# Kernel tuning notes

Measured on AMD Instinct MI355X. Metric: run time of the kernel, lower is better.

The kernel has to match this reference:

```python
import jax, jax.numpy as jnp
import numpy as np

N_NODES = 20000
N_EDGES = 640000
IN_DIM = 256
HID = 128
N_GRAPHS = 64


def setup_inputs() -> dict:
    key = jax.random.key(0)
    ks = jax.random.split(key, 9)
    x = jax.random.normal(ks[0], (N_NODES, IN_DIM), jnp.float32)
    edge_index = jax.random.randint(ks[1], (2, N_EDGES), 0, N_NODES, dtype=jnp.int32)
    batch = jnp.sort(jax.random.randint(ks[2], (N_NODES,), 0, N_GRAPHS, dtype=jnp.int32))

    def lin(k, fan_in, fan_out):
        # torch.nn.Linear default init: U(-1/sqrt(fan_in), 1/sqrt(fan_in))
        bound = 1.0 / np.sqrt(fan_in)
        kw, kb = jax.random.split(k)
        W = jax.random.uniform(kw, (fan_in, fan_out), jnp.float32, -bound, bound)
        b = jax.random.uniform(kb, (fan_out,), jnp.float32, -bound, bound)
        return W, b

    W0, b0 = lin(ks[3], IN_DIM, HID)
    W1, b1 = lin(ks[4], HID, HID)
    W2, b2 = lin(ks[5], HID, HID)
    return dict(x=x, edge_index=edge_index, batch=batch,
                W0=W0, b0=b0, W1=W1, b1=b1, W2=W2, b2=b2)


def reference(x, edge_index, batch, W0, b0, W1, b1, W2, b2):
    src, dst = edge_index[0], edge_index[1]
    edge_batch = batch[src]  # [E] segment id per edge
    ones = jnp.ones((edge_batch.shape[0], 1), x.dtype)
    counts = jax.ops.segment_sum(ones, edge_batch, num_segments=N_GRAPHS)
    inv_counts = 1.0 / jnp.maximum(counts, 1.0)

    def pool(z):
        # gather endpoint features, concat -> [E, 2*HID], mean pool by graph
        edge_emb = jnp.concatenate([z[src], z[dst]], axis=1)
        return jax.ops.segment_sum(edge_emb, edge_batch, num_segments=N_GRAPHS) * inv_counts

    g = []
    z = x
    for W, b in ((W0, b0), (W1, b1), (W2, b2)):
        z = z @ W + b
        g.append(pool(z))
    return jnp.concatenate(g, axis=1)  # [N_GRAPHS, 3 * 2 * HID]
```

## Files before the change

kernel.cpp:

```cpp
#include <hip/hip_runtime.h>

#define N_NODES 20000
#define N_EDGES 640000
#define N_GRAPHS 64

#define NCHUNK 256
#define CHUNK_SZ 79
#define GSPLIT 8
#define GSUB 8

#define BG_TILE 2048
#define NBG 313
#define SEGCAP 80
#define GR_CAP 768
#define NSLOT4 (NBG * SEGCAP / 4)

#define CD_OFF      0
#define DEG_OFF     1280000
#define CNT_OFF     1300000
#define Y_OFF       1300064
#define PART_OFF    1316448
#define BH_OFF      5510752
#define VALS_OFF    5530784

__global__ __launch_bounds__(256) void bucket_g_k(const int* __restrict__ ei,
                                                  const int* __restrict__ batch,
                                                  unsigned* __restrict__ vals,
                                                  unsigned* __restrict__ bh,
                                                  float* __restrict__ Y) {
    __shared__ unsigned hist[N_GRAPHS];
    __shared__ unsigned base[N_GRAPHS + 1];
    __shared__ unsigned lv[BG_TILE];
    __shared__ unsigned char gidx[BG_TILE];
    const int t = threadIdx.x;
    const int blk = blockIdx.x;
    if (t < N_GRAPHS) hist[t] = 0u;
    __syncthreads();

    const int e0 = blk * BG_TILE;
    const int ecnt = (e0 + BG_TILE <= N_EDGES) ? BG_TILE : (N_EDGES - e0);
    unsigned pv[8], rnk[8], gg[8];
#pragma unroll
    for (int k = 0; k < 8; ++k) {
        int i = t + k * 256;
        if (i < ecnt) {
            unsigned s = (unsigned)ei[e0 + i];
            unsigned d = (unsigned)ei[N_EDGES + e0 + i];
            unsigned g = (unsigned)batch[s];
            pv[k] = (s << 15) | d;
            gg[k] = g;
            rnk[k] = atomicAdd(&hist[g], 1u);
        } else {
            gg[k] = 0xFFFFFFFFu;
        }
    }
    __syncthreads();
    if (t == 0) {
        unsigned acc = 0u;
        base[0] = 0u;
        for (int g = 0; g < N_GRAPHS; ++g) { acc += hist[g]; base[g + 1] = acc; }
    }
    if (t < N_GRAPHS) {
        unsigned c = hist[t];
        bh[blk * N_GRAPHS + t] = (c > SEGCAP) ? SEGCAP : c;
    }
    __syncthreads();
    if (t < N_GRAPHS) {
        unsigned b0 = base[t], b1 = base[t + 1];
        for (unsigned i = b0; i < b1; ++i) gidx[i] = (unsigned char)t;
    }
#pragma unroll
    for (int k = 0; k < 8; ++k) {
        if (gg[k] != 0xFFFFFFFFu) lv[base[gg[k]] + rnk[k]] = pv[k];
    }
    __syncthreads();
    for (int i = t; i < ecnt; i += 256) {
        unsigned g = gidx[i];
        unsigned slot = (unsigned)i - base[g];
        if (slot < SEGCAP)
            vals[((size_t)g * NBG + blk) * SEGCAP + slot] = lv[i];
    }
    if (blk == 0) {
        float4* y4 = (float4*)Y;
        for (int i = t; i < 64 * 64; i += 256) y4[i] = make_float4(0.f, 0.f, 0.f, 0.f);
    }
}

__global__ __launch_bounds__(1024) void cd_col_k(const unsigned* __restrict__ vals,
                                                 const unsigned* __restrict__ bh,
                                                 const int* __restrict__ batch,
                                                 float* __restrict__ Cdcol,
                                                 float* __restrict__ deg,
                                                 float* __restrict__ counts) {
    __shared__ unsigned scnt[NBG];
    __shared__ unsigned dh[2500];
    __shared__ unsigned sdeg[GR_CAP];
    __shared__ int s_lo, s_hi;
    const int t = threadIdx.x;
    const int g = blockIdx.x >> 2;
    const int q = blockIdx.x & 3;
    const int d0 = q * 5000;

    for (int i = t; i < 2500; i += 1024) dh[i] = 0u;
    if (t < NBG) scnt[t] = bh[t * N_GRAPHS + g];
    if (q == 0) {
        if (t < GR_CAP) sdeg[t] = 0u;
        if (t == 0) {
            int lo = 0, hi = N_NODES;
            while (lo < hi) { int m = (lo + hi) >> 1; if (batch[m] < g) lo = m + 1; else hi = m; }
            s_lo = lo;
            int lo2 = lo; hi = N_NODES;
            while (lo2 < hi) { int m = (lo2 + hi) >> 1; if (batch[m] < g + 1) lo2 = m + 1; else hi = m; }
            s_hi = lo2;
        }
    }
    __syncthreads();
    const int lo = (q == 0) ? s_lo : 0;

    const uint4* v4 = (const uint4*)(vals + (size_t)g * NBG * SEGCAP);
    for (int i = t; i < NSLOT4; i += 1024) {
        uint4 v = *(v4 + i);
        unsigned w = (unsigned)i * 4u;
        unsigned seg = (unsigned)(((unsigned long long)w * 53687092ull) >> 32);
        unsigned local = w - seg * 80u;
        unsigned c = scnt[seg];
#define CD_ONE(VX, L)                                                            \
        if ((L) < c) {                                                           \
            int rd_ = (int)((VX) & 0x7FFFu) - d0;                                \
            if ((unsigned)rd_ < 5000u)                                           \
                atomicAdd(&dh[rd_ >> 1], 1u << ((rd_ & 1) * 16));                \
            if (q == 0) {                                                        \
                int rs_ = (int)((VX) >> 15) - lo;                                \
                if ((unsigned)rs_ < (unsigned)GR_CAP) atomicAdd(&sdeg[rs_], 1u); \
            }                                                                    \
        }
        CD_ONE(v.x, local + 0u)
        CD_ONE(v.y, local + 1u)
        CD_ONE(v.z, local + 2u)
        CD_ONE(v.w, local + 3u)
#undef CD_ONE
    }
    __syncthreads();

    float2* outc = (float2*)(Cdcol + (size_t)g * N_NODES + d0);
    for (int w = t; w < 2500; w += 1024) {
        unsigned v = dh[w];
        outc[w] = make_float2((float)(v & 0xFFFFu), (float)(v >> 16));
    }
    if (q == 0) {
        const int range = s_hi - lo;
        for (int i = t; i < range; i += 1024) deg[lo + i] = (float)sdeg[i];
        if (t == 0) {
            unsigned tot = 0;
            for (int i = 0; i < NBG; ++i) tot += scnt[i];
            counts[g] = (float)tot;
        }
    }
}

#define FMA8(C0, C1, XV)                                          \
    acc[0].x = fmaf(C0.x, XV.x, acc[0].x); acc[0].y = fmaf(C0.x, XV.y, acc[0].y); \
    acc[0].z = fmaf(C0.x, XV.z, acc[0].z); acc[0].w = fmaf(C0.x, XV.w, acc[0].w); \
    acc[1].x = fmaf(C0.y, XV.x, acc[1].x); acc[1].y = fmaf(C0.y, XV.y, acc[1].y); \
    acc[1].z = fmaf(C0.y, XV.z, acc[1].z); acc[1].w = fmaf(C0.y, XV.w, acc[1].w); \
    acc[2].x = fmaf(C0.z, XV.x, acc[2].x); acc[2].y = fmaf(C0.z, XV.y, acc[2].y); \
    acc[2].z = fmaf(C0.z, XV.z, acc[2].z); acc[2].w = fmaf(C0.z, XV.w, acc[2].w); \
    acc[3].x = fmaf(C0.w, XV.x, acc[3].x); acc[3].y = fmaf(C0.w, XV.y, acc[3].y); \
    acc[3].z = fmaf(C0.w, XV.z, acc[3].z); acc[3].w = fmaf(C0.w, XV.w, acc[3].w); \
    acc[4].x = fmaf(C1.x, XV.x, acc[4].x); acc[4].y = fmaf(C1.x, XV.y, acc[4].y); \
    acc[4].z = fmaf(C1.x, XV.z, acc[4].z); acc[4].w = fmaf(C1.x, XV.w, acc[4].w); \
    acc[5].x = fmaf(C1.y, XV.x, acc[5].x); acc[5].y = fmaf(C1.y, XV.y, acc[5].y); \
    acc[5].z = fmaf(C1.y, XV.z, acc[5].z); acc[5].w = fmaf(C1.y, XV.w, acc[5].w); \
    acc[6].x = fmaf(C1.z, XV.x, acc[6].x); acc[6].y = fmaf(C1.z, XV.y, acc[6].y); \
    acc[6].z = fmaf(C1.z, XV.z, acc[6].z); acc[6].w = fmaf(C1.z, XV.w, acc[6].w); \
    acc[7].x = fmaf(C1.w, XV.x, acc[7].x); acc[7].y = fmaf(C1.w, XV.y, acc[7].y); \
    acc[7].z = fmaf(C1.w, XV.z, acc[7].z); acc[7].w = fmaf(C1.w, XV.w, acc[7].w);

__global__ __launch_bounds__(256) void pool_k(const float* __restrict__ x,
                                              const int* __restrict__ batch,
                                              const float* __restrict__ Cdcol,
                                              const float* __restrict__ deg,
                                              float* __restrict__ Y,
                                              float* __restrict__ part) {
    __shared__ float4 sc4[CHUNK_SZ * 2];
    __shared__ float sdeg[CHUNK_SZ];
    __shared__ int   sbatch[CHUNK_SZ];
    __shared__ float4 red[2 * GSUB * 64];

    const int t = threadIdx.x;
    const int fg = t & 63;
    const int p  = t >> 6;
    const int b = blockIdx.x & 255;
    const int j = blockIdx.x >> 8;
    const int n0 = b * CHUNK_SZ;
    int cnt = N_NODES - n0;
    if (cnt > CHUNK_SZ) cnt = CHUNK_SZ;
    if (cnt < 0) cnt = 0;

    float* sc = (float*)sc4;
    const float* cbase = Cdcol + (size_t)(j * GSUB) * N_NODES + n0;
#pragma unroll
    for (int k = 0; k < GSUB; ++k)
        for (int i = t; i < cnt; i += 256)
            sc[i * GSUB + k] = cbase[(size_t)k * N_NODES + i];
    if (j == 0) {
        for (int i = t; i < cnt; i += 256) {
            sdeg[i] = deg[n0 + i];
            sbatch[i] = batch[n0 + i];
        }
    }
    __syncthreads();

    const float4* xp = (const float4*)x + (size_t)n0 * 64 + fg;
#define XL(I) xp[(size_t)(I) * 64]
    float4 acc[GSUB];
#pragma unroll
    for (int k = 0; k < GSUB; ++k) acc[k] = make_float4(0.f, 0.f, 0.f, 0.f);

    if (j == 0) {
        float4 accs = make_float4(0.f, 0.f, 0.f, 0.f);
        int gprev = (p < cnt) ? sbatch[p] : 0;
        int i = p;
        float4 xn = make_float4(0.f, 0.f, 0.f, 0.f);
        if (i < cnt) xn = XL(i);
        for (; i < cnt; i += 4) {
            float4 xv = xn;
            if (i + 4 < cnt) xn = XL(i + 4);
            int g = sbatch[i];
            if (g != gprev) {
                float* yr = Y + gprev * 256 + fg * 4;
                atomicAdd(yr + 0, accs.x); atomicAdd(yr + 1, accs.y);
                atomicAdd(yr + 2, accs.z); atomicAdd(yr + 3, accs.w);
                accs = make_float4(0.f, 0.f, 0.f, 0.f);
                gprev = g;
            }
            float dg = sdeg[i];
            accs.x = fmaf(dg, xv.x, accs.x); accs.y = fmaf(dg, xv.y, accs.y);
            accs.z = fmaf(dg, xv.z, accs.z); accs.w = fmaf(dg, xv.w, accs.w);
            float4 c0 = sc4[i * 2], c1 = sc4[i * 2 + 1];
            FMA8(c0, c1, xv)
        }
        if (p < cnt) {
            float* yr = Y + gprev * 256 + fg * 4;
            atomicAdd(yr + 0, accs.x); atomicAdd(yr + 1, accs.y);
            atomicAdd(yr + 2, accs.z); atomicAdd(yr + 3, accs.w);
        }
    } else {
        int i = p;
        float4 xa, xb;
        if (i     < cnt) xa = XL(i);
        if (i + 4 < cnt) xb = XL(i + 4);
        for (; i + 4 < cnt; i += 8) {
            float4 y0 = xa, y1 = xb;
            if (i + 8  < cnt) xa = XL(i + 8);
            if (i + 12 < cnt) xb = XL(i + 12);
            { float4 c0 = sc4[i * 2],       c1 = sc4[i * 2 + 1];       FMA8(c0, c1, y0) }
            { float4 c0 = sc4[(i + 4) * 2], c1 = sc4[(i + 4) * 2 + 1]; FMA8(c0, c1, y1) }
        }
        for (; i < cnt; i += 4) {
            float4 xv = XL(i);
            float4 c0 = sc4[i * 2], c1 = sc4[i * 2 + 1];
            FMA8(c0, c1, xv)
        }
    }
#undef XL

    if (p >= 2) {
#pragma unroll
        for (int k = 0; k < GSUB; ++k) red[(p - 2) * (GSUB * 64) + k * 64 + fg] = acc[k];
    }
    __syncthreads();
    if (p < 2) {
#pragma unroll
        for (int k = 0; k < GSUB; ++k) {
            float4 v = red[p * (GSUB * 64) + k * 64 + fg];
            acc[k].x += v.x; acc[k].y += v.y; acc[k].z += v.z; acc[k].w += v.w;
        }
    }
    __syncthreads();
    if (p == 1) {
#pragma unroll
        for (int k = 0; k < GSUB; ++k) red[k * 64 + fg] = acc[k];
    }
    __syncthreads();
    if (p == 0) {
        float4* part4 = (float4*)part;
#pragma unroll
        for (int k = 0; k < GSUB; ++k) {
            float4 v = red[k * 64 + fg];
            acc[k].x += v.x; acc[k].y += v.y; acc[k].z += v.z; acc[k].w += v.w;
            part4[(size_t)(b * 64 + j * GSUB + k) * 64 + fg] = acc[k];
        }
    }
}

__global__ __launch_bounds__(256) void chain2_k(const float* __restrict__ Y,
                                                const float* __restrict__ part,
                                                const float* __restrict__ counts,
                                                const float* __restrict__ W0, const float* __restrict__ b0,
                                                const float* __restrict__ W1, const float* __restrict__ b1,
                                                const float* __restrict__ W2, const float* __restrict__ b2,
                                                float* __restrict__ out) {
    __shared__ float m[256];
    __shared__ float h[128];
    const int r = blockIdx.x;
    const int t = threadIdx.x;
    const int g = r & 63;
    const int half = (r >= 64) ? 128 : 0;

    float c = counts[g];
    float inv = 1.0f / fmaxf(c, 1.0f);
    float beta = c * inv;

    if (r < 64) {
        m[t] = Y[r * 256 + t] * inv;
    } else {
        float s = 0.0f;
        for (int bb = 0; bb < NCHUNK; ++bb) s += part[(size_t)(bb * 64 + g) * 256 + t];
        m[t] = s * inv;
    }
    __syncthreads();

    if (t < 128) {
        float s1 = 0.0f;
        for (int k = 0; k < 256; ++k) s1 += m[k] * W0[k * 128 + t];
        s1 += beta * b0[t];
        out[g * 768 + 0 + half + t] = s1;
        h[t] = s1;
    }
    __syncthreads();
    float s2 = 0.0f;
    if (t < 128) {
        for (int k = 0; k < 128; ++k) s2 += h[k] * W1[k * 128 + t];
        s2 += beta * b1[t];
        out[g * 768 + 256 + half + t] = s2;
    }
    __syncthreads();
    if (t < 128) h[t] = s2;
    __syncthreads();
    if (t < 128) {
        float s3 = 0.0f;
        for (int k = 0; k < 128; ++k) s3 += h[k] * W2[k * 128 + t];
        s3 += beta * b2[t];
        out[g * 768 + 512 + half + t] = s3;
    }
}

extern "C" void kernel_launch(void* const* d_in, const int* in_sizes, int n_in,
                              void* d_out, int out_size, void* d_ws, size_t ws_size,
                              hipStream_t stream) {
    const float* x     = (const float*)d_in[0];
    const int*   ei    = (const int*)d_in[1];
    const int*   batch = (const int*)d_in[2];
    const float* W0    = (const float*)d_in[3];
    const float* b0    = (const float*)d_in[4];
    const float* W1    = (const float*)d_in[5];
    const float* b1    = (const float*)d_in[6];
    const float* W2    = (const float*)d_in[7];
    const float* b2    = (const float*)d_in[8];
    float* out = (float*)d_out;

    float*    ws     = (float*)d_ws;
    float*    Cdcol  = ws + CD_OFF;
    float*    deg    = ws + DEG_OFF;
    float*    counts = ws + CNT_OFF;
    float*    Y      = ws + Y_OFF;
    float*    part   = ws + PART_OFF;
    unsigned* bh     = (unsigned*)(ws + BH_OFF);
    unsigned* vals   = (unsigned*)(ws + VALS_OFF);

    bucket_g_k<<<NBG, 256, 0, stream>>>(ei, batch, vals, bh, Y);
    cd_col_k<<<N_GRAPHS * 4, 1024, 0, stream>>>(vals, bh, batch, Cdcol, deg, counts);
    pool_k<<<NCHUNK * GSPLIT, 256, 0, stream>>>(x, batch, Cdcol, deg, Y, part);
    chain2_k<<<128, 256, 0, stream>>>(Y, part, counts, W0, b0, W1, b1, W2, b2, out);
}
```

Measured before the change: 130.0 us.

## Fuse four kernels into one persistent cooperative kernel with grid syncs

Replaces the four separate launches (bucketing, degree/count histogram, pooling, final MLP chain) with one cooperative persistent kernel that loops over jobs and separates phases with grid.sync(). The bucketing and histogram phases are re-tiled to smaller tiles (1024 edge blocks, 16 destination slices per graph) so they fit 256-thread blocks. The intent is to remove inter-kernel launch gaps and tail effects. In exchange it adds grid-wide barrier costs, and the grid is sized from an occupancy query, which may leave some phases underparallelised. The old four-kernel path is kept as a fallback if the cooperative launch fails.

Measured after the change: 378.0 us. 191% more time.

```diff
diff --git a/kernel.cpp b/kernel.cpp
--- a/kernel.cpp
+++ b/kernel.cpp
@@ -1,4 +1,6 @@
 #include <hip/hip_runtime.h>
+#include <hip/hip_cooperative_groups.h>
+namespace cg = cooperative_groups;
 
 #define N_NODES 20000
 #define N_EDGES 640000
@@ -8,12 +10,18 @@
 #define CHUNK_SZ 79
 #define GSPLIT 8
 #define GSUB 8
+#define NPOOLJOB (NCHUNK * GSPLIT)
 
 #define BG_TILE 2048
 #define NBG 313
 #define SEGCAP 80
 #define GR_CAP 768
 #define NSLOT4 (NBG * SEGCAP / 4)
+
+#define FNBLK 1024
+#define FBTILE 625
+#define FSEGCAP 48
+#define FNSLOT4 (FNBLK * FSEGCAP / 4)
 
 #define CD_OFF      0
 #define DEG_OFF     1280000
@@ -22,141 +30,8 @@
 #define PART_OFF    1316448
 #define BH_OFF      5510752
 #define VALS_OFF    5530784
-
-__global__ __launch_bounds__(256) void bucket_g_k(const int* __restrict__ ei,
-                                                  const int* __restrict__ batch,
-                                                  unsigned* __restrict__ vals,
-                                                  unsigned* __restrict__ bh,
-                                                  float* __restrict__ Y) {
-    __shared__ unsigned hist[N_GRAPHS];
-    __shared__ unsigned base[N_GRAPHS + 1];
-    __shared__ unsigned lv[BG_TILE];
-    __shared__ unsigned char gidx[BG_TILE];
-    const int t = threadIdx.x;
-    const int blk = blockIdx.x;
-    if (t < N_GRAPHS) hist[t] = 0u;
-    __syncthreads();
-
-    const int e0 = blk * BG_TILE;
-    const int ecnt = (e0 + BG_TILE <= N_EDGES) ? BG_TILE : (N_EDGES - e0);
-    unsigned pv[8], rnk[8], gg[8];
-#pragma unroll
-    for (int k = 0; k < 8; ++k) {
-        int i = t + k * 256;
-        if (i < ecnt) {
-            unsigned s = (unsigned)ei[e0 + i];
-            unsigned d = (unsigned)ei[N_EDGES + e0 + i];
-            unsigned g = (unsigned)batch[s];
-            pv[k] = (s << 15) | d;
-            gg[k] = g;
-            rnk[k] = atomicAdd(&hist[g], 1u);
-        } else {
-            gg[k] = 0xFFFFFFFFu;
-        }
-    }
-    __syncthreads();
-    if (t == 0) {
-        unsigned acc = 0u;
-        base[0] = 0u;
-        for (int g = 0; g < N_GRAPHS; ++g) { acc += hist[g]; base[g + 1] = acc; }
-    }
-    if (t < N_GRAPHS) {
-        unsigned c = hist[t];
-        bh[blk * N_GRAPHS + t] = (c > SEGCAP) ? SEGCAP : c;
-    }
-    __syncthreads();
-    if (t < N_GRAPHS) {
-        unsigned b0 = base[t], b1 = base[t + 1];
-        for (unsigned i = b0; i < b1; ++i) gidx[i] = (unsigned char)t;
-    }
-#pragma unroll
-    for (int k = 0; k < 8; ++k) {
-        if (gg[k] != 0xFFFFFFFFu) lv[base[gg[k]] + rnk[k]] = pv[k];
-    }
-    __syncthreads();
-    for (int i = t; i < ecnt; i += 256) {
-        unsigned g = gidx[i];
-        unsigned slot = (unsigned)i - base[g];
-        if (slot < SEGCAP)
-            vals[((size_t)g * NBG + blk) * SEGCAP + slot] = lv[i];
-    }
-    if (blk == 0) {
-        float4* y4 = (float4*)Y;
-        for (int i = t; i < 64 * 64; i += 256) y4[i] = make_float4(0.f, 0.f, 0.f, 0.f);
-    }
-}
-
-__global__ __launch_bounds__(1024) void cd_col_k(const unsigned* __restrict__ vals,
-                                                 const unsigned* __restrict__ bh,
-                                                 const int* __restrict__ batch,
-                                                 float* __restrict__ Cdcol,
-                                                 float* __restrict__ deg,
-                                                 float* __restrict__ counts) {
-    __shared__ unsigned scnt[NBG];
-    __shared__ unsigned dh[2500];
-    __shared__ unsigned sdeg[GR_CAP];
-    __shared__ int s_lo, s_hi;
-    const int t = threadIdx.x;
-    const int g = blockIdx.x >> 2;
-    const int q = blockIdx.x & 3;
-    const int d0 = q * 5000;
-
-    for (int i = t; i < 2500; i += 1024) dh[i] = 0u;
-    if (t < NBG) scnt[t] = bh[t * N_GRAPHS + g];
-    if (q == 0) {
-        if (t < GR_CAP) sdeg[t] = 0u;
-        if (t == 0) {
-            int lo = 0, hi = N_NODES;
-            while (lo < hi) { int m = (lo + hi) >> 1; if (batch[m] < g) lo = m + 1; else hi = m; }
-            s_lo = lo;
-            int lo2 = lo; hi = N_NODES;
-            while (lo2 < hi) { int m = (lo2 + hi) >> 1; if (batch[m] < g + 1) lo2 = m + 1; else hi = m; }
-            s_hi = lo2;
-        }
-    }
-    __syncthreads();
-    const int lo = (q == 0) ? s_lo : 0;
-
-    const uint4* v4 = (const uint4*)(vals + (size_t)g * NBG * SEGCAP);
-    for (int i = t; i < NSLOT4; i += 1024) {
-        uint4 v = *(v4 + i);
-        unsigned w = (unsigned)i * 4u;
-        unsigned seg = (unsigned)(((unsigned long long)w * 53687092ull) >> 32);
-        unsigned local = w - seg * 80u;
-        unsigned c = scnt[seg];
-#define CD_ONE(VX, L)                                                            \
-        if ((L) < c) {                                                           \
-            int rd_ = (int)((VX) & 0x7FFFu) - d0;                                \
-            if ((unsigned)rd_ < 5000u)                                           \
-                atomicAdd(&dh[rd_ >> 1], 1u << ((rd_ & 1) * 16));                \
-            if (q == 0) {                                                        \
-                int rs_ = (int)((VX) >> 15) - lo;                                \
-                if ((unsigned)rs_ < (unsigned)GR_CAP) atomicAdd(&sdeg[rs_], 1u); \
-            }                                                                    \
-        }
-        CD_ONE(v.x, local + 0u)
-        CD_ONE(v.y, local + 1u)
-        CD_ONE(v.z, local + 2u)
-        CD_ONE(v.w, local + 3u)
-#undef CD_ONE
-    }
-    __syncthreads();
-
-    float2* outc = (float2*)(Cdcol + (size_t)g * N_NODES + d0);
-    for (int w = t; w < 2500; w += 1024) {
-        unsigned v = dh[w];
-        outc[w] = make_float2((float)(v & 0xFFFFu), (float)(v >> 16));
-    }
-    if (q == 0) {
-        const int range = s_hi - lo;
-        for (int i = t; i < range; i += 1024) deg[lo + i] = (float)sdeg[i];
-        if (t == 0) {
-            unsigned tot = 0;
-            for (int i = 0; i < NBG; ++i) tot += scnt[i];
-            counts[g] = (float)tot;
-        }
-    }
-}
+#define BH2_OFF     8000000
+#define VALS2_OFF   8065536
 
 #define FMA8(C0, C1, XV)                                          \
     acc[0].x = fmaf(C0.x, XV.x, acc[0].x); acc[0].y = fmaf(C0.x, XV.y, acc[0].y); \
@@ -176,6 +51,427 @@
     acc[7].x = fmaf(C1.w, XV.x, acc[7].x); acc[7].y = fmaf(C1.w, XV.y, acc[7].y); \
     acc[7].z = fmaf(C1.w, XV.z, acc[7].z); acc[7].w = fmaf(C1.w, XV.w, acc[7].w);
 
+__global__ void fused_k(const float* __restrict__ x,
+                        const int* __restrict__ ei,
+                        const int* __restrict__ batch,
+                        const float* __restrict__ W0, const float* __restrict__ b0,
+                        const float* __restrict__ W1, const float* __restrict__ b1,
+                        const float* __restrict__ W2, const float* __restrict__ b2,
+                        float* __restrict__ out,
+                        float* __restrict__ Cdcol, float* __restrict__ deg,
+                        float* __restrict__ counts, float* __restrict__ Y,
+                        float* __restrict__ part,
+                        unsigned* __restrict__ bh2, unsigned* __restrict__ vals2) {
+    cg::grid_group grid = cg::this_grid();
+    const int t = threadIdx.x;
+    const int blk = blockIdx.x;
+    const int gsz = (int)gridDim.x;
+
+    __shared__ unsigned hist[N_GRAPHS];
+    __shared__ unsigned base[N_GRAPHS + 1];
+    __shared__ unsigned lv[FBTILE];
+    __shared__ unsigned char gidx[FBTILE + 3];
+    for (int job = blk; job < FNBLK; job += gsz) {
+        __syncthreads();
+        if (t < N_GRAPHS) hist[t] = 0u;
+        __syncthreads();
+        const int e0 = job * FBTILE;
+        unsigned pv[3], rnk[3], gg[3];
+#pragma unroll
+        for (int k = 0; k < 3; ++k) {
+            int i = t + k * 256;
+            if (i < FBTILE) {
+                unsigned s = (unsigned)ei[e0 + i];
+                unsigned d = (unsigned)ei[N_EDGES + e0 + i];
+                unsigned g = (unsigned)batch[s];
+                pv[k] = (s << 15) | d;
+                gg[k] = g;
+                rnk[k] = atomicAdd(&hist[g], 1u);
+            } else gg[k] = 0xFFFFFFFFu;
+        }
+        __syncthreads();
+        if (t == 0) {
+            unsigned a = 0u; base[0] = 0u;
+            for (int g = 0; g < N_GRAPHS; ++g) { a += hist[g]; base[g + 1] = a; }
+        }
+        if (t < N_GRAPHS) {
+            unsigned c = hist[t];
+            bh2[job * N_GRAPHS + t] = (c > FSEGCAP) ? FSEGCAP : c;
+        }
+        __syncthreads();
+        if (t < N_GRAPHS) {
+            for (unsigned i = base[t]; i < base[t + 1]; ++i) gidx[i] = (unsigned char)t;
+        }
+#pragma unroll
+        for (int k = 0; k < 3; ++k)
+            if (gg[k] != 0xFFFFFFFFu) lv[base[gg[k]] + rnk[k]] = pv[k];
+        __syncthreads();
+        for (int i = t; i < FBTILE; i += 256) {
+            unsigned g = gidx[i];
+            unsigned slot = (unsigned)i - base[g];
+            if (slot < FSEGCAP)
+                vals2[(size_t)g * (FNBLK * FSEGCAP) + (unsigned)job * FSEGCAP + slot] = lv[i];
+        }
+        if (job == 0) {
+            float4* y4 = (float4*)Y;
+            for (int i = t; i < 64 * 64; i += 256) y4[i] = make_float4(0.f, 0.f, 0.f, 0.f);
+        }
+    }
+    grid.sync();
+
+    __shared__ unsigned scnt2[FNBLK];
+    __shared__ unsigned dh2[625];
+    __shared__ unsigned sdeg2[GR_CAP];
+    __shared__ int s_lo, s_hi;
+    for (int job = blk; job < FNBLK; job += gsz) {
+        __syncthreads();
+        const int g = job >> 4;
+        const int six = job & 15;
+        const int d0 = six * 1250;
+        for (int i = t; i < FNBLK; i += 256) scnt2[i] = bh2[i * N_GRAPHS + g];
+        for (int i = t; i < 625; i += 256) dh2[i] = 0u;
+        if (six == 0) {
+            for (int i = t; i < GR_CAP; i += 256) sdeg2[i] = 0u;
+            if (t == 0) {
+                int lo = 0, hi = N_NODES;
+                while (lo < hi) { int m = (lo + hi) >> 1; if (batch[m] < g) lo = m + 1; else hi = m; }
+                s_lo = lo;
+                int lo2 = lo; hi = N_NODES;
+                while (lo2 < hi) { int m = (lo2 + hi) >> 1; if (batch[m] < g + 1) lo2 = m + 1; else hi = m; }
+                s_hi = lo2;
+            }
+        }
+        __syncthreads();
+        const int lo = (six == 0) ? s_lo : 0;
+        const uint4* v4 = (const uint4*)(vals2 + (size_t)g * (FNBLK * FSEGCAP));
+        for (int i = t; i < FNSLOT4; i += 256) {
+            uint4 v = v4[i];
+            unsigned w = (unsigned)i * 4u;
+            unsigned seg = w / FSEGCAP;
+            unsigned local = w - seg * FSEGCAP;
+            unsigned c = scnt2[seg];
+#define CD_ONE(VX, L)                                                             \
+            if ((L) < c) {                                                        \
+                int rd_ = (int)((VX) & 0x7FFFu) - d0;                             \
+                if ((unsigned)rd_ < 1250u)                                        \
+                    atomicAdd(&dh2[rd_ >> 1], 1u << ((rd_ & 1) * 16));            \
+                if (six == 0) {                                                   \
+                    int rs_ = (int)((VX) >> 15) - lo;                             \
+                    if ((unsigned)rs_ < (unsigned)GR_CAP) atomicAdd(&sdeg2[rs_], 1u); \
+                }                                                                 \
+            }
+            CD_ONE(v.x, local + 0u)
+            CD_ONE(v.y, local + 1u)
+            CD_ONE(v.z, local + 2u)
+            CD_ONE(v.w, local + 3u)
+#undef CD_ONE
+        }
+        __syncthreads();
+        float2* outc = (float2*)(Cdcol + (size_t)g * N_NODES + d0);
+        for (int w = t; w < 625; w += 256) {
+            unsigned v = dh2[w];
+            outc[w] = make_float2((float)(v & 0xFFFFu), (float)(v >> 16));
+        }
+        if (six == 0) {
+            const int range = s_hi - lo;
+            for (int i = t; i < range; i += 256) deg[lo + i] = (float)sdeg2[i];
+            if (t == 0) {
+                unsigned tot = 0;
+                for (int i = 0; i < FNBLK; ++i) tot += scnt2[i];
+                counts[g] = (float)tot;
+            }
+        }
+    }
+    grid.sync();
+
+    __shared__ float4 sc4[CHUNK_SZ * 2];
+    __shared__ float sdeg[CHUNK_SZ];
+    __shared__ int   sbatch[CHUNK_SZ];
+    __shared__ float4 red[2 * GSUB * 64];
+    const int fg = t & 63;
+    const int p  = t >> 6;
+    for (int job = blk; job < NPOOLJOB; job += gsz) {
+        __syncthreads();
+        const int b = job & 255;
+        const int j = job >> 8;
+        const int n0 = b * CHUNK_SZ;
+        int cnt = N_NODES - n0;
+        if (cnt > CHUNK_SZ) cnt = CHUNK_SZ;
+        if (cnt < 0) cnt = 0;
+
+        float* sc = (float*)sc4;
+        const float* cbase = Cdcol + (size_t)(j * GSUB) * N_NODES + n0;
+#pragma unroll
+        for (int k = 0; k < GSUB; ++k)
+            for (int i = t; i < cnt; i += 256)
+                sc[i * GSUB + k] = cbase[(size_t)k * N_NODES + i];
+        if (j == 0) {
+            for (int i = t; i < cnt; i += 256) {
+                sdeg[i] = deg[n0 + i];
+                sbatch[i] = batch[n0 + i];
+            }
+        }
+        __syncthreads();
+
+        const float4* xp = (const float4*)x + (size_t)n0 * 64 + fg;
+#define XL(I) xp[(size_t)(I) * 64]
+        float4 acc[GSUB];
+#pragma unroll
+        for (int k = 0; k < GSUB; ++k) acc[k] = make_float4(0.f, 0.f, 0.f, 0.f);
+
+        if (j == 0) {
+            float4 accs = make_float4(0.f, 0.f, 0.f, 0.f);
+            int gprev = (p < cnt) ? sbatch[p] : 0;
+            int i = p;
+            float4 xn = make_float4(0.f, 0.f, 0.f, 0.f);
+            if (i < cnt) xn = XL(i);
+            for (; i < cnt; i += 4) {
+                float4 xv = xn;
+                if (i + 4 < cnt) xn = XL(i + 4);
+                int g = sbatch[i];
+                if (g != gprev) {
+                    float* yr = Y + gprev * 256 + fg * 4;
+                    atomicAdd(yr + 0, accs.x); atomicAdd(yr + 1, accs.y);
+                    atomicAdd(yr + 2, accs.z); atomicAdd(yr + 3, accs.w);
+                    accs = make_float4(0.f, 0.f, 0.f, 0.f);
+                    gprev = g;
+                }
+                float dg = sdeg[i];
+                accs.x = fmaf(dg, xv.x, accs.x); accs.y = fmaf(dg, xv.y, accs.y);
+                accs.z = fmaf(dg, xv.z, accs.z); accs.w = fmaf(dg, xv.w, accs.w);
+                float4 c0 = sc4[i * 2], c1 = sc4[i * 2 + 1];
+                FMA8(c0, c1, xv)
+            }
+            if (p < cnt) {
+                float* yr = Y + gprev * 256 + fg * 4;
+                atomicAdd(yr + 0, accs.x); atomicAdd(yr + 1, accs.y);
+                atomicAdd(yr + 2, accs.z); atomicAdd(yr + 3, accs.w);
+            }
+        } else {
+            int i = p;
+            float4 xa, xb;
+            if (i     < cnt) xa = XL(i);
+            if (i + 4 < cnt) xb = XL(i + 4);
+            for (; i + 4 < cnt; i += 8) {
+                float4 y0 = xa, y1 = xb;
+                if (i + 8  < cnt) xa = XL(i + 8);
+                if (i + 12 < cnt) xb = XL(i + 12);
+                { float4 c0 = sc4[i * 2],       c1 = sc4[i * 2 + 1];       FMA8(c0, c1, y0) }
+                { float4 c0 = sc4[(i + 4) * 2], c1 = sc4[(i + 4) * 2 + 1]; FMA8(c0, c1, y1) }
+            }
+            for (; i < cnt; i += 4) {
+                float4 xv = XL(i);
+                float4 c0 = sc4[i * 2], c1 = sc4[i * 2 + 1];
+                FMA8(c0, c1, xv)
+            }
+        }
+#undef XL
+
+        if (p >= 2) {
+#pragma unroll
+            for (int k = 0; k < GSUB; ++k) red[(p - 2) * (GSUB * 64) + k * 64 + fg] = acc[k];
+        }
+        __syncthreads();
+        if (p < 2) {
+#pragma unroll
+            for (int k = 0; k < GSUB; ++k) {
+                float4 v = red[p * (GSUB * 64) + k * 64 + fg];
+                acc[k].x += v.x; acc[k].y += v.y; acc[k].z += v.z; acc[k].w += v.w;
+            }
+        }
+        __syncthreads();
+        if (p == 1) {
+#pragma unroll
+            for (int k = 0; k < GSUB; ++k) red[k * 64 + fg] = acc[k];
+        }
+        __syncthreads();
+        if (p == 0) {
+            float4* part4 = (float4*)part;
+#pragma unroll
+            for (int k = 0; k < GSUB; ++k) {
+                float4 v = red[k * 64 + fg];
+                acc[k].x += v.x; acc[k].y += v.y; acc[k].z += v.z; acc[k].w += v.w;
+                part4[(size_t)(b * 64 + j * GSUB + k) * 64 + fg] = acc[k];
+            }
+        }
+    }
+    grid.sync();
+
+    __shared__ float m2[256];
+    __shared__ float h2[128];
+    for (int job = blk; job < 128; job += gsz) {
+        __syncthreads();
+        const int r = job;
+        const int g = r & 63;
+        const int half = (r >= 64) ? 128 : 0;
+        float c = counts[g];
+        float inv = 1.0f / fmaxf(c, 1.0f);
+        float beta = c * inv;
+
+        if (r < 64) {
+            m2[t] = Y[r * 256 + t] * inv;
+        } else {
+            float s = 0.0f;
+            for (int bb = 0; bb < NCHUNK; ++bb) s += part[(size_t)(bb * 64 + g) * 256 + t];
+            m2[t] = s * inv;
+        }
+        __syncthreads();
+        if (t < 128) {
+            float s1 = 0.0f;
+            for (int k = 0; k < 256; ++k) s1 += m2[k] * W0[k * 128 + t];
+            s1 += beta * b0[t];
+            out[g * 768 + 0 + half + t] = s1;
+            h2[t] = s1;
+        }
+        __syncthreads();
+        float s2 = 0.0f;
+        if (t < 128) {
+            for (int k = 0; k < 128; ++k) s2 += h2[k] * W1[k * 128 + t];
+            s2 += beta * b1[t];
+            out[g * 768 + 256 + half + t] = s2;
+        }
+        __syncthreads();
+        if (t < 128) h2[t] = s2;
+        __syncthreads();
+        if (t < 128) {
+            float s3 = 0.0f;
+            for (int k = 0; k < 128; ++k) s3 += h2[k] * W2[k * 128 + t];
+            s3 += beta * b2[t];
+            out[g * 768 + 512 + half + t] = s3;
+        }
+    }
+}
+
+__global__ __launch_bounds__(256) void bucket_g_k(const int* __restrict__ ei,
+                                                  const int* __restrict__ batch,
+                                                  unsigned* __restrict__ vals,
+                                                  unsigned* __restrict__ bh,
+                                                  float* __restrict__ Y) {
+    __shared__ unsigned hist[N_GRAPHS];
+    __shared__ unsigned base[N_GRAPHS + 1];
+    __shared__ unsigned lv[BG_TILE];
+    __shared__ unsigned char gidx[BG_TILE];
+    const int t = threadIdx.x;
+    const int blk = blockIdx.x;
+    if (t < N_GRAPHS) hist[t] = 0u;
+    __syncthreads();
+
+    const int e0 = blk * BG_TILE;
+    const int ecnt = (e0 + BG_TILE <= N_EDGES) ? BG_TILE : (N_EDGES - e0);
+    unsigned pv[8], rnk[8], gg[8];
+#pragma unroll
+    for (int k = 0; k < 8; ++k) {
+        int i = t + k * 256;
+        if (i < ecnt) {
+            unsigned s = (unsigned)ei[e0 + i];
+            unsigned d = (unsigned)ei[N_EDGES + e0 + i];
+            unsigned g = (unsigned)batch[s];
+            pv[k] = (s << 15) | d;
+            gg[k] = g;
+            rnk[k] = atomicAdd(&hist[g], 1u);
+        } else gg[k] = 0xFFFFFFFFu;
+    }
+    __syncthreads();
+    if (t == 0) {
+        unsigned a = 0u; base[0] = 0u;
+        for (int g = 0; g < N_GRAPHS; ++g) { a += hist[g]; base[g + 1] = a; }
+    }
+    if (t < N_GRAPHS) {
+        unsigned c = hist[t];
+        bh[blk * N_GRAPHS + t] = (c > SEGCAP) ? SEGCAP : c;
+    }
+    __syncthreads();
+    if (t < N_GRAPHS) {
+        for (unsigned i = base[t]; i < base[t + 1]; ++i) gidx[i] = (unsigned char)t;
+    }
+#pragma unroll
+    for (int k = 0; k < 8; ++k)
+        if (gg[k] != 0xFFFFFFFFu) lv[base[gg[k]] + rnk[k]] = pv[k];
+    __syncthreads();
+    for (int i = t; i < ecnt; i += 256) {
+        unsigned g = gidx[i];
+        unsigned slot = (unsigned)i - base[g];
+        if (slot < SEGCAP)
+            vals[((size_t)g * NBG + blk) * SEGCAP + slot] = lv[i];
+    }
+    if (blk == 0) {
+        float4* y4 = (float4*)Y;
+        for (int i = t; i < 64 * 64; i += 256) y4[i] = make_float4(0.f, 0.f, 0.f, 0.f);
+    }
+}
+
+__global__ __launch_bounds__(1024) void cd_col_k(const unsigned* __restrict__ vals,
+                                                 const unsigned* __restrict__ bh,
+                                                 const int* __restrict__ batch,
+                                                 float* __restrict__ Cdcol,
+                                                 float* __restrict__ deg,
+                                                 float* __restrict__ counts) {
+    __shared__ unsigned scnt[NBG];
+    __shared__ unsigned dh[2500];
+    __shared__ unsigned sdeg[GR_CAP];
+    __shared__ int s_lo, s_hi;
+    const int t = threadIdx.x;
+    const int g = blockIdx.x >> 2;
+    const int q = blockIdx.x & 3;
+    const int d0 = q * 5000;
+
+    for (int i = t; i < 2500; i += 1024) dh[i] = 0u;
+    if (t < NBG) scnt[t] = bh[t * N_GRAPHS + g];
+    if (q == 0) {
+        if (t < GR_CAP) sdeg[t] = 0u;
+        if (t == 0) {
+            int lo = 0, hi = N_NODES;
+            while (lo < hi) { int m = (lo + hi) >> 1; if (batch[m] < g) lo = m + 1; else hi = m; }
+            s_lo = lo;
+            int lo2 = lo; hi = N_NODES;
+            while (lo2 < hi) { int m = (lo2 + hi) >> 1; if (batch[m] < g + 1) lo2 = m + 1; else hi = m; }
+            s_hi = lo2;
+        }
+    }
+    __syncthreads();
+    const int lo = (q == 0) ? s_lo : 0;
+
+    const uint4* v4 = (const uint4*)(vals + (size_t)g * NBG * SEGCAP);
+    for (int i = t; i < NSLOT4; i += 1024) {
+        uint4 v = *(v4 + i);
+        unsigned w = (unsigned)i * 4u;
+        unsigned seg = w / SEGCAP;
+        unsigned local = w - seg * SEGCAP;
+        unsigned c = scnt[seg];
+#define CD_ONE(VX, L)                                                            \
+        if ((L) < c) {                                                           \
+            int rd_ = (int)((VX) & 0x7FFFu) - d0;                                \
+            if ((unsigned)rd_ < 5000u)                                           \
+                atomicAdd(&dh[rd_ >> 1], 1u << ((rd_ & 1) * 16));                \
+            if (q == 0) {                                                        \
+                int rs_ = (int)((VX) >> 15) - lo;                                \
+                if ((unsigned)rs_ < (unsigned)GR_CAP) atomicAdd(&sdeg[rs_], 1u); \
+            }                                                                    \
+        }
+        CD_ONE(v.x, local + 0u)
+        CD_ONE(v.y, local + 1u)
+        CD_ONE(v.z, local + 2u)
+        CD_ONE(v.w, local + 3u)
+#undef CD_ONE
+    }
+    __syncthreads();
+
+    float2* outc = (float2*)(Cdcol + (size_t)g * N_NODES + d0);
+    for (int w = t; w < 2500; w += 1024) {
+        unsigned v = dh[w];
+        outc[w] = make_float2((float)(v & 0xFFFFu), (float)(v >> 16));
+    }
+    if (q == 0) {
+        const int range = s_hi - lo;
+        for (int i = t; i < range; i += 1024) deg[lo + i] = (float)sdeg[i];
+        if (t == 0) {
+            unsigned tot = 0;
+            for (int i = 0; i < NBG; ++i) tot += scnt[i];
+            counts[g] = (float)tot;
+        }
+    }
+}
+
 __global__ __launch_bounds__(256) void pool_k(const float* __restrict__ x,
                                               const int* __restrict__ batch,
                                               const float* __restrict__ Cdcol,
@@ -368,9 +664,28 @@
     float*    part   = ws + PART_OFF;
     unsigned* bh     = (unsigned*)(ws + BH_OFF);
     unsigned* vals   = (unsigned*)(ws + VALS_OFF);
-
-    bucket_g_k<<<NBG, 256, 0, stream>>>(ei, batch, vals, bh, Y);
-    cd_col_k<<<N_GRAPHS * 4, 1024, 0, stream>>>(vals, bh, batch, Cdcol, deg, counts);
-    pool_k<<<NCHUNK * GSPLIT, 256, 0, stream>>>(x, batch, Cdcol, deg, Y, part);
-    chain2_k<<<128, 256, 0, stream>>>(Y, part, counts, W0, b0, W1, b1, W2, b2, out);
+    unsigned* bh2    = (unsigned*)(ws + BH2_OFF);
+    unsigned* vals2  = (unsigned*)(ws + VALS2_OFF);
+
+    int occ = 0;
+    hipError_t qe = hipOccupancyMaxActiveBlocksPerMultiprocessor(&occ, (const void*)fused_k, 256, 0);
+    bool coop_ok = false;
+    if (qe == hipSuccess && occ > 0) {
+        int grid = occ * 256;
+        if (grid > NPOOLJOB) grid = NPOOLJOB;
+        void* args[] = { (void*)&x, (void*)&ei, (void*)&batch,
+                         (void*)&W0, (void*)&b0, (void*)&W1, (void*)&b1,
+                         (void*)&W2, (void*)&b2, (void*)&out,
+                         (void*)&Cdcol, (void*)&deg, (void*)&counts, (void*)&Y,
+                         (void*)&part, (void*)&bh2, (void*)&vals2 };
+        hipError_t le = hipLaunchCooperativeKernel((void*)fused_k, dim3(grid), dim3(256),
+                                                   args, 0, stream);
+        coop_ok = (le == hipSuccess);
+    }
+    if (!coop_ok) {
+        bucket_g_k<<<NBG, 256, 0, stream>>>(ei, batch, vals, bh, Y);
+        cd_col_k<<<N_GRAPHS * 4, 1024, 0, stream>>>(vals, bh, batch, Cdcol, deg, counts);
+        pool_k<<<NCHUNK * GSPLIT, 256, 0, stream>>>(x, batch, Cdcol, deg, Y, part);
+        chain2_k<<<128, 256, 0, stream>>>(Y, part, counts, W0, b0, W1, b1, W2, b2, out);
+    }
 }
```
